# Performance work log

Hardware: AMD Instinct MI355X
Metric: run time of the kernel (lower is better)

## Reference

```python
import jax, jax.numpy as jnp
import numpy as np

ALPHA = 0.5
NEG_INF_DIAG = 1e6


def setup_inputs() -> dict:
    key = jax.random.key(0)
    k1, k2, k3, k4 = jax.random.split(key, 4)
    B, Nq, Ns, D = 64, 32, 1024, 128
    return {
        "query_single": jax.random.normal(k1, (B, D), dtype=jnp.float32),
        "doc_single": jax.random.normal(k2, (B, D), dtype=jnp.float32),
        "query_multi": jax.random.normal(k3, (B, Nq, D), dtype=jnp.float32),
        "doc_multi": jax.random.normal(k4, (B, Ns, D), dtype=jnp.float32),
    }


def _single_vector_loss(q, d):
    # q, d: (B, D) -> in-batch softmax cross-entropy with diagonal targets
    scores = jnp.einsum("bd,cd->bc", q, d)  # (B, B)
    logp = jax.nn.log_softmax(scores, axis=-1)
    return -jnp.mean(jnp.diagonal(logp))


def _multi_vector_loss(q, d):
    # q: (B, Nq, D), d: (B, Ns, D)
    # MaxSim: max over doc tokens, sum over query tokens
    sim = jnp.einsum("bnd,csd->bcns", q, d)  # (B, B, Nq, Ns) -- large intermediate
    scores = jnp.sum(jnp.max(sim, axis=3), axis=2)  # (B, B)
    pos = jnp.diagonal(scores)  # (B,)
    B = scores.shape[0]
    neg = jnp.max(scores - jnp.eye(B, dtype=scores.dtype) * NEG_INF_DIAG, axis=1)
    return jnp.mean(jax.nn.softplus(neg - pos))


def reference(query_single, doc_single, query_multi, doc_multi):
    sv_loss = _single_vector_loss(query_single, doc_single)
    mv_loss = _multi_vector_loss(query_multi, doc_multi)
    total = ALPHA * sv_loss + (1.0 - ALPHA) * mv_loss
    return sv_loss, mv_loss, total
```

## Files before the change

### kernel.cpp

```cpp
#include <hip/hip_runtime.h>


typedef __attribute__((ext_vector_type(8))) short short8;
typedef __attribute__((ext_vector_type(4))) float f32x4;

static __device__ __forceinline__ unsigned short f2bf(float f) {
  unsigned int u = __float_as_uint(f);
  u += 0x7fffu + ((u >> 16) & 1u);
  return (unsigned short)(u >> 16);
}

static __device__ __forceinline__ void g2l16(const void* g, void* l) {
  __builtin_amdgcn_global_load_lds(
      (const __attribute__((address_space(1))) unsigned int*)g,
      (__attribute__((address_space(3))) unsigned int*)l, 16, 0, 0);
}

__global__ void convert_kernel(const float* __restrict__ qm,
                               const float* __restrict__ dm,
                               unsigned char* __restrict__ dmb,
                               unsigned short* __restrict__ qmb) {
  const int NDM = 1048576;
  const int NT = NDM + 32768;
  for (int g = blockIdx.x * 256 + threadIdx.x; g < NT;
       g += gridDim.x * 256) {
    const float* src;
    unsigned char* dst;
    if (g < NDM) {
      const int c = g >> 14;
      const int r = g & 16383;
      const int s = r >> 4;
      const int kc = r & 15;
      src = dm + ((size_t)c * 131072 + (size_t)s * 128 + kc * 8);
      dst = dmb + ((size_t)c * 262144 + s * 256 +
                   ((kc * 16) ^ ((s & 7) << 4)));
    } else {
      const int gg = g - NDM;
      const int row = gg >> 4;
      const int kc = gg & 15;
      src = qm + (size_t)row * 128 + kc * 8;
      dst = (unsigned char*)(qmb + (size_t)row * 128 + kc * 8);
    }
    const float4 a = *(const float4*)src;
    const float4 b = *(const float4*)(src + 4);
    short8 w;
    w[0] = (short)f2bf(a.x); w[1] = (short)f2bf(a.y);
    w[2] = (short)f2bf(a.z); w[3] = (short)f2bf(a.w);
    w[4] = (short)f2bf(b.x); w[5] = (short)f2bf(b.y);
    w[6] = (short)f2bf(b.z); w[7] = (short)f2bf(b.w);
    *(short8*)dst = w;
  }
}

__global__ __launch_bounds__(256, 2) void mv_kernel(
    const unsigned short* __restrict__ qmb,
    const unsigned char* __restrict__ dmb,
    const float* __restrict__ qs, const float* __restrict__ ds,
    float* __restrict__ part, float* __restrict__ svp) {
  __shared__ __align__(16) unsigned char smem[34816];

  const int tid = threadIdx.x;
  const int ln = tid & 63;
  const int wv = tid >> 6;
  const int wgid = blockIdx.x;

  if (wgid >= 512) {
    const int rb = wgid - 512;
    float* dl = (float*)smem;
    for (int i = tid; i < 8192; i += 256)
      dl[(i >> 7) * 129 + (i & 127)] = ds[i];
    __syncthreads();
    const int cc = ln;
    for (int rr = 0; rr < 2; ++rr) {
      const int row = rb * 8 + wv * 2 + rr;
      const float* q = qs + (size_t)row * 128;
      float acc = 0.f;
#pragma unroll
      for (int k = 0; k < 128; ++k) acc += q[k] * dl[cc * 129 + k];
      float m = acc;
      for (int d = 1; d < 64; d <<= 1) m = fmaxf(m, __shfl_xor(m, d));
      float e = expf(acc - m);
      float ssum = e;
      for (int d = 1; d < 64; d <<= 1) ssum += __shfl_xor(ssum, d);
      const float lp = acc - m - logf(ssum);
      const float diag = __shfl(lp, row);
      if (ln == 0) svp[row] = -diag;
    }
    return;
  }

  const int rb = wgid & 3;
  const int c = (wgid >> 2) & 63;
  const int sc = wgid >> 8;

  const int lrow = ln & 15;
  const int lkg = ln >> 4;

  short8 qf[8][4];
#pragma unroll
  for (int rt = 0; rt < 8; ++rt) {
    const int row = rb * 512 + wv * 128 + rt * 16 + lrow;
    const unsigned short* qp = qmb + (size_t)row * 128 + lkg * 8;
#pragma unroll
    for (int kk = 0; kk < 4; ++kk)
      qf[rt][kk] = *(const short8*)(qp + kk * 32);
  }

  f32x4 maxv[8];
#pragma unroll
  for (int rt = 0; rt < 8; ++rt)
#pragma unroll
    for (int r = 0; r < 4; ++r) maxv[rt][r] = -3.0e38f;

  const unsigned char* dbase = dmb + (size_t)c * 262144 + (size_t)sc * 131072;
  float* rowmax = (float*)(smem + 32768);

#pragma unroll
  for (int i = 0; i < 4; ++i) {
    const int chunk = wv * 4 + i;
    g2l16(dbase + chunk * 1024 + ln * 16, smem + chunk * 1024);
  }
  __syncthreads();

  for (int t = 0; t < 8; ++t) {
    const unsigned char* cur = smem + (t & 1) * 16384;
    if (t < 7) {
      unsigned char* nxt = smem + ((t + 1) & 1) * 16384;
      const unsigned char* gsrc = dbase + (t + 1) * 16384;
#pragma unroll
      for (int i = 0; i < 4; ++i) {
        const int chunk = wv * 4 + i;
        g2l16(gsrc + chunk * 1024 + ln * 16, nxt + chunk * 1024);
      }
    }
#pragma unroll
    for (int cc = 0; cc < 4; ++cc) {
      const int s = cc * 16 + lrow;
      const unsigned char* bp = cur + s * 256;
      const int swz = (s & 7) << 4;
      short8 df[4];
#pragma unroll
      for (int kk = 0; kk < 4; ++kk)
        df[kk] = *(const short8*)(bp + ((kk * 64 + lkg * 16) ^ swz));
#pragma unroll
      for (int rt = 0; rt < 8; ++rt) {
        f32x4 a = {0.f, 0.f, 0.f, 0.f};
#pragma unroll
        for (int kk = 0; kk < 4; ++kk)
          a = __builtin_amdgcn_mfma_f32_16x16x32_bf16(qf[rt][kk], df[kk], a,
                                                      0, 0, 0);
#pragma unroll
        for (int r = 0; r < 4; ++r) maxv[rt][r] = fmaxf(maxv[rt][r], a[r]);
      }
    }
    __syncthreads();
  }

#pragma unroll
  for (int rt = 0; rt < 8; ++rt)
#pragma unroll
    for (int r = 0; r < 4; ++r) {
      float v = maxv[rt][r];
      v = fmaxf(v, __shfl_xor(v, 1));
      v = fmaxf(v, __shfl_xor(v, 2));
      v = fmaxf(v, __shfl_xor(v, 4));
      v = fmaxf(v, __shfl_xor(v, 8));
      if (lrow == 0) rowmax[wv * 128 + rt * 16 + lkg * 4 + r] = v;
    }
  __syncthreads();

  const size_t pb = (size_t)(c * 2 + sc) * 2048 + rb * 512;
  part[pb + tid] = rowmax[tid];
  part[pb + 256 + tid] = rowmax[256 + tid];
}

__global__ void reduce_kernel(const float* __restrict__ part,
                              float* __restrict__ scores) {
  const int c = blockIdx.x;
  const int t = threadIdx.x;
  const float* p0 = part + (size_t)(c * 2 + 0) * 2048;
  const float* p1 = part + (size_t)(c * 2 + 1) * 2048;
  float s = 0.f;
#pragma unroll
  for (int i = 0; i < 8; ++i) {
    const int r = t * 8 + i;
    s += fmaxf(p0[r], p1[r]);
  }
  s += __shfl_xor(s, 1);
  s += __shfl_xor(s, 2);
  if ((t & 3) == 0) scores[(t >> 2) * 64 + c] = s;
}

__global__ void final_kernel(const float* __restrict__ scores,
                             const float* __restrict__ svp,
                             float* __restrict__ out) {
  const int b = threadIdx.x;
  float sv = svp[b];
  for (int d = 1; d < 64; d <<= 1) sv += __shfl_xor(sv, d);
  sv *= (1.0f / 64.0f);

  const float pos = scores[b * 64 + b];
  float neg = -3.0e38f;
  for (int c = 0; c < 64; ++c) {
    float v = scores[b * 64 + c] - (c == b ? 1.0e6f : 0.0f);
    neg = fmaxf(neg, v);
  }
  const float t = neg - pos;
  float sp = fmaxf(t, 0.f) + log1pf(expf(-fabsf(t)));
  for (int d = 1; d < 64; d <<= 1) sp += __shfl_xor(sp, d);
  if (b == 0) {
    const float mvl = sp / 64.0f;
    out[0] = sv;
    out[1] = mvl;
    out[2] = 0.5f * sv + 0.5f * mvl;
  }
}

__global__ void sv_kernel_fb(const float* __restrict__ qs,
                             const float* __restrict__ ds,
                             float* __restrict__ out_sv) {
  __shared__ float sc[64][64];
  const int tid = threadIdx.x;
  for (int p = tid; p < 4096; p += 256) {
    const int b = p >> 6, c = p & 63;
    const float4* qa = (const float4*)(qs + b * 128);
    const float4* da = (const float4*)(ds + c * 128);
    float acc = 0.f;
#pragma unroll
    for (int i = 0; i < 32; ++i) {
      const float4 x = qa[i], y = da[i];
      acc += x.x * y.x + x.y * y.y + x.z * y.z + x.w * y.w;
    }
    sc[b][c] = acc;
  }
  __syncthreads();
  if (tid < 64) {
    float m = -3.0e38f;
    for (int c = 0; c < 64; ++c) m = fmaxf(m, sc[tid][c]);
    float s = 0.f;
    for (int c = 0; c < 64; ++c) s += expf(sc[tid][c] - m);
    float lp = sc[tid][tid] - (m + logf(s));
    for (int d = 1; d < 64; d <<= 1) lp += __shfl_xor(lp, d);
    if (tid == 0) *out_sv = -lp / 64.0f;
  }
}

__global__ __launch_bounds__(256, 4) void mv_gemm_fb(
    const float* __restrict__ qm, const float* __restrict__ dm,
    float* __restrict__ scores) {
  __shared__ unsigned char dtb[64 * 256];
  __shared__ float rowmax[128];
  const int c = blockIdx.y;
  const int rb = blockIdx.x;
  const int tid = threadIdx.x;
  const int ln = tid & 63;
  const int wv = tid >> 6;
  const int lrow = ln & 15;
  const int lkg = ln >> 4;
  short8 qf[2][4];
#pragma unroll
  for (int rt = 0; rt < 2; ++rt) {
    const int row = rb * 128 + wv * 32 + rt * 16 + lrow;
    const float* qp = qm + (size_t)row * 128 + lkg * 8;
#pragma unroll
    for (int kk = 0; kk < 4; ++kk) {
      const float4 a = *(const float4*)(qp + kk * 32);
      const float4 b = *(const float4*)(qp + kk * 32 + 4);
      short8 f;
      f[0] = (short)f2bf(a.x); f[1] = (short)f2bf(a.y);
      f[2] = (short)f2bf(a.z); f[3] = (short)f2bf(a.w);
      f[4] = (short)f2bf(b.x); f[5] = (short)f2bf(b.y);
      f[6] = (short)f2bf(b.z); f[7] = (short)f2bf(b.w);
      qf[rt][kk] = f;
    }
  }
  f32x4 maxv[2];
#pragma unroll
  for (int rt = 0; rt < 2; ++rt)
#pragma unroll
    for (int r = 0; r < 4; ++r) maxv[rt][r] = -3.0e38f;
  const float* dbase = dm + (size_t)c * 1024 * 128;
  for (int t = 0; t < 16; ++t) {
    __syncthreads();
#pragma unroll
    for (int i = 0; i < 4; ++i) {
      const int ch = tid + i * 256;
      const int s = ch >> 4;
      const int kc = ch & 15;
      const float* p = dbase + (size_t)(t * 64 + s) * 128 + kc * 8;
      const float4 a = *(const float4*)p;
      const float4 b = *(const float4*)(p + 4);
      short8 w;
      w[0] = (short)f2bf(a.x); w[1] = (short)f2bf(a.y);
      w[2] = (short)f2bf(a.z); w[3] = (short)f2bf(a.w);
      w[4] = (short)f2bf(b.x); w[5] = (short)f2bf(b.y);
      w[6] = (short)f2bf(b.z); w[7] = (short)f2bf(b.w);
      *(short8*)(dtb + s * 256 + ((kc * 16) ^ ((s & 7) << 4))) = w;
    }
    __syncthreads();
#pragma unroll
    for (int cc = 0; cc < 4; ++cc) {
      const int s = cc * 16 + lrow;
      short8 df[4];
#pragma unroll
      for (int kk = 0; kk < 4; ++kk)
        df[kk] = *(const short8*)(dtb + s * 256 +
                                  ((kk * 64 + lkg * 16) ^ ((s & 7) << 4)));
#pragma unroll
      for (int rt = 0; rt < 2; ++rt) {
        f32x4 acc = {0.f, 0.f, 0.f, 0.f};
#pragma unroll
        for (int kk = 0; kk < 4; ++kk)
          acc = __builtin_amdgcn_mfma_f32_16x16x32_bf16(qf[rt][kk], df[kk],
                                                        acc, 0, 0, 0);
#pragma unroll
        for (int r = 0; r < 4; ++r) maxv[rt][r] = fmaxf(maxv[rt][r], acc[r]);
      }
    }
  }
#pragma unroll
  for (int rt = 0; rt < 2; ++rt)
#pragma unroll
    for (int r = 0; r < 4; ++r) {
      float v = maxv[rt][r];
      v = fmaxf(v, __shfl_xor(v, 1));
      v = fmaxf(v, __shfl_xor(v, 2));
      v = fmaxf(v, __shfl_xor(v, 4));
      v = fmaxf(v, __shfl_xor(v, 8));
      maxv[rt][r] = v;
    }
  if (lrow == 0) {
#pragma unroll
    for (int rt = 0; rt < 2; ++rt)
#pragma unroll
      for (int r = 0; r < 4; ++r)
        rowmax[wv * 32 + rt * 16 + lkg * 4 + r] = maxv[rt][r];
  }
  __syncthreads();
  if (tid < 128) {
    float v = rowmax[tid];
    v += __shfl_xor(v, 1);
    v += __shfl_xor(v, 2);
    v += __shfl_xor(v, 4);
    v += __shfl_xor(v, 8);
    v += __shfl_xor(v, 16);
    if ((tid & 31) == 0) scores[(rb * 4 + (tid >> 5)) * 64 + c] = v;
  }
}

__global__ void final_fb(const float* __restrict__ scores,
                         const float* __restrict__ sv_ptr,
                         float* __restrict__ out) {
  const int b = threadIdx.x;
  const float pos = scores[b * 64 + b];
  float neg = -3.0e38f;
  for (int c = 0; c < 64; ++c) {
    float v = scores[b * 64 + c] - (c == b ? 1.0e6f : 0.0f);
    neg = fmaxf(neg, v);
  }
  const float t = neg - pos;
  float sp = fmaxf(t, 0.f) + log1pf(expf(-fabsf(t)));
  for (int d = 1; d < 64; d <<= 1) sp += __shfl_xor(sp, d);
  if (b == 0) {
    const float mvl = sp / 64.0f;
    const float sv = *sv_ptr;
    out[0] = sv;
    out[1] = mvl;
    out[2] = 0.5f * sv + 0.5f * mvl;
  }
}

extern "C" void kernel_launch(void* const* d_in, const int* in_sizes, int n_in,
                              void* d_out, int out_size, void* d_ws,
                              size_t ws_size, hipStream_t stream) {
  const float* qs = (const float*)d_in[0];
  const float* ds = (const float*)d_in[1];
  const float* qm = (const float*)d_in[2];
  const float* dm = (const float*)d_in[3];
  float* out = (float*)d_out;

  const size_t NEED = 16777216u + 524288u + 1048576u + 16384u + 256u;
  if (ws_size >= NEED) {
    unsigned char* dmb = (unsigned char*)d_ws;
    unsigned short* qmb = (unsigned short*)(dmb + 16777216u);
    float* part = (float*)(dmb + 16777216u + 524288u);
    float* scores = (float*)(dmb + 16777216u + 524288u + 1048576u);
    float* svp = scores + 4096;
    convert_kernel<<<2048, 256, 0, stream>>>(qm, dm, dmb, qmb);
    mv_kernel<<<520, 256, 0, stream>>>(qmb, dmb, qs, ds, part, svp);
    reduce_kernel<<<64, 256, 0, stream>>>(part, scores);
    final_kernel<<<1, 64, 0, stream>>>(scores, svp, out);
  } else {
    float* scores = (float*)d_ws;
    float* sv = scores + 4096;
    sv_kernel_fb<<<1, 256, 0, stream>>>(qs, ds, sv);
    mv_gemm_fb<<<dim3(16, 64), 256, 0, stream>>>(qm, dm, scores);
    final_fb<<<1, 64, 0, stream>>>(scores, sv, out);
  }
}
```

Baseline: 55.23 us.

## Fuse fp32-to-bf16 conversion into MaxSim kernel, dropping separate convert pass

Removes the standalone convert kernel that wrote a bf16 swizzled copy of the doc and query tensors to workspace. The main kernel now streams fp32 doc tiles into LDS, converts them to a bf16 swizzled double buffer in-kernel, and converts the query fragments in registers on load. This saves a kernel launch and a full write-plus-reread of the bf16 copy. In exchange each workgroup reads twice the bytes per tile, uses about 66KB of LDS (which may lower occupancy), and adds an extra barrier plus conversion work per tile.

Result: slower. 185.3 us (+235.6%).

```diff
diff --git a/kernel.cpp b/kernel.cpp
--- a/kernel.cpp
+++ b/kernel.cpp
@@ -16,48 +16,11 @@
       (__attribute__((address_space(3))) unsigned int*)l, 16, 0, 0);
 }
 
-__global__ void convert_kernel(const float* __restrict__ qm,
-                               const float* __restrict__ dm,
-                               unsigned char* __restrict__ dmb,
-                               unsigned short* __restrict__ qmb) {
-  const int NDM = 1048576;
-  const int NT = NDM + 32768;
-  for (int g = blockIdx.x * 256 + threadIdx.x; g < NT;
-       g += gridDim.x * 256) {
-    const float* src;
-    unsigned char* dst;
-    if (g < NDM) {
-      const int c = g >> 14;
-      const int r = g & 16383;
-      const int s = r >> 4;
-      const int kc = r & 15;
-      src = dm + ((size_t)c * 131072 + (size_t)s * 128 + kc * 8);
-      dst = dmb + ((size_t)c * 262144 + s * 256 +
-                   ((kc * 16) ^ ((s & 7) << 4)));
-    } else {
-      const int gg = g - NDM;
-      const int row = gg >> 4;
-      const int kc = gg & 15;
-      src = qm + (size_t)row * 128 + kc * 8;
-      dst = (unsigned char*)(qmb + (size_t)row * 128 + kc * 8);
-    }
-    const float4 a = *(const float4*)src;
-    const float4 b = *(const float4*)(src + 4);
-    short8 w;
-    w[0] = (short)f2bf(a.x); w[1] = (short)f2bf(a.y);
-    w[2] = (short)f2bf(a.z); w[3] = (short)f2bf(a.w);
-    w[4] = (short)f2bf(b.x); w[5] = (short)f2bf(b.y);
-    w[6] = (short)f2bf(b.z); w[7] = (short)f2bf(b.w);
-    *(short8*)dst = w;
-  }
-}
-
 __global__ __launch_bounds__(256, 2) void mv_kernel(
-    const unsigned short* __restrict__ qmb,
-    const unsigned char* __restrict__ dmb,
+    const float* __restrict__ qm, const float* __restrict__ dm,
     const float* __restrict__ qs, const float* __restrict__ ds,
     float* __restrict__ part, float* __restrict__ svp) {
-  __shared__ __align__(16) unsigned char smem[34816];
+  __shared__ __align__(16) unsigned char smem[67584];
 
   const int tid = threadIdx.x;
   const int ln = tid & 63;
@@ -96,14 +59,33 @@
   const int lrow = ln & 15;
   const int lkg = ln >> 4;
 
+  float* fbuf = (float*)smem;
+  float* rowmax = (float*)(smem + 65536);
+
+  const float* dmF = dm + (size_t)c * 131072 + (size_t)sc * 65536;
+
+#pragma unroll
+  for (int i = 0; i < 8; ++i) {
+    const int ch = wv * 8 + i;
+    g2l16(dmF + ch * 256 + ln * 4, smem + ch * 1024 + ln * 16);
+  }
+
   short8 qf[8][4];
 #pragma unroll
   for (int rt = 0; rt < 8; ++rt) {
     const int row = rb * 512 + wv * 128 + rt * 16 + lrow;
-    const unsigned short* qp = qmb + (size_t)row * 128 + lkg * 8;
-#pragma unroll
-    for (int kk = 0; kk < 4; ++kk)
-      qf[rt][kk] = *(const short8*)(qp + kk * 32);
+    const float* qp = qm + (size_t)row * 128 + lkg * 8;
+#pragma unroll
+    for (int kk = 0; kk < 4; ++kk) {
+      const float4 a = *(const float4*)(qp + kk * 32);
+      const float4 b = *(const float4*)(qp + kk * 32 + 4);
+      short8 f;
+      f[0] = (short)f2bf(a.x); f[1] = (short)f2bf(a.y);
+      f[2] = (short)f2bf(a.z); f[3] = (short)f2bf(a.w);
+      f[4] = (short)f2bf(b.x); f[5] = (short)f2bf(b.y);
+      f[6] = (short)f2bf(b.z); f[7] = (short)f2bf(b.w);
+      qf[rt][kk] = f;
+    }
   }
 
   f32x4 maxv[8];
@@ -112,27 +94,38 @@
 #pragma unroll
     for (int r = 0; r < 4; ++r) maxv[rt][r] = -3.0e38f;
 
-  const unsigned char* dbase = dmb + (size_t)c * 262144 + (size_t)sc * 131072;
-  float* rowmax = (float*)(smem + 32768);
-
-#pragma unroll
-  for (int i = 0; i < 4; ++i) {
-    const int chunk = wv * 4 + i;
-    g2l16(dbase + chunk * 1024 + ln * 16, smem + chunk * 1024);
-  }
   __syncthreads();
 
+  {
+    unsigned char* bb = smem + 32768;
+#pragma unroll
+    for (int i = 0; i < 4; ++i) {
+      const int ch = tid + i * 256;
+      const int s = ch >> 4;
+      const int kc = ch & 15;
+      const float* p = fbuf + s * 128 + kc * 8;
+      const float4 a = *(const float4*)p;
+      const float4 b = *(const float4*)(p + 4);
+      short8 w;
+      w[0] = (short)f2bf(a.x); w[1] = (short)f2bf(a.y);
+      w[2] = (short)f2bf(a.z); w[3] = (short)f2bf(a.w);
+      w[4] = (short)f2bf(b.x); w[5] = (short)f2bf(b.y);
+      w[6] = (short)f2bf(b.z); w[7] = (short)f2bf(b.w);
+      *(short8*)(bb + s * 256 + ((kc * 16) ^ ((s & 7) << 4))) = w;
+    }
+  }
+
   for (int t = 0; t < 8; ++t) {
-    const unsigned char* cur = smem + (t & 1) * 16384;
+    __syncthreads();
     if (t < 7) {
-      unsigned char* nxt = smem + ((t + 1) & 1) * 16384;
-      const unsigned char* gsrc = dbase + (t + 1) * 16384;
-#pragma unroll
-      for (int i = 0; i < 4; ++i) {
-        const int chunk = wv * 4 + i;
-        g2l16(gsrc + chunk * 1024 + ln * 16, nxt + chunk * 1024);
+      const float* gt = dmF + (t + 1) * 8192;
+#pragma unroll
+      for (int i = 0; i < 8; ++i) {
+        const int ch = wv * 8 + i;
+        g2l16(gt + ch * 256 + ln * 4, smem + ch * 1024 + ln * 16);
       }
     }
+    const unsigned char* cur = smem + 32768 + (t & 1) * 16384;
 #pragma unroll
     for (int cc = 0; cc < 4; ++cc) {
       const int s = cc * 16 + lrow;
@@ -154,6 +147,24 @@
       }
     }
     __syncthreads();
+    if (t < 7) {
+      unsigned char* bb = smem + 32768 + ((t + 1) & 1) * 16384;
+#pragma unroll
+      for (int i = 0; i < 4; ++i) {
+        const int ch = tid + i * 256;
+        const int s = ch >> 4;
+        const int kc = ch & 15;
+        const float* p = fbuf + s * 128 + kc * 8;
+        const float4 a = *(const float4*)p;
+        const float4 b = *(const float4*)(p + 4);
+        short8 w;
+        w[0] = (short)f2bf(a.x); w[1] = (short)f2bf(a.y);
+        w[2] = (short)f2bf(a.z); w[3] = (short)f2bf(a.w);
+        w[4] = (short)f2bf(b.x); w[5] = (short)f2bf(b.y);
+        w[6] = (short)f2bf(b.z); w[7] = (short)f2bf(b.w);
+        *(short8*)(bb + s * 256 + ((kc * 16) ^ ((s & 7) << 4))) = w;
+      }
+    }
   }
 
 #pragma unroll
@@ -379,15 +390,12 @@
   const float* dm = (const float*)d_in[3];
   float* out = (float*)d_out;
 
-  const size_t NEED = 16777216u + 524288u + 1048576u + 16384u + 256u;
+  const size_t NEED = 1048576u + 16384u + 256u;
   if (ws_size >= NEED) {
-    unsigned char* dmb = (unsigned char*)d_ws;
-    unsigned short* qmb = (unsigned short*)(dmb + 16777216u);
-    float* part = (float*)(dmb + 16777216u + 524288u);
-    float* scores = (float*)(dmb + 16777216u + 524288u + 1048576u);
+    float* part = (float*)d_ws;
+    float* scores = (float*)((unsigned char*)d_ws + 1048576u);
     float* svp = scores + 4096;
-    convert_kernel<<<2048, 256, 0, stream>>>(qm, dm, dmb, qmb);
-    mv_kernel<<<520, 256, 0, stream>>>(qmb, dmb, qs, ds, part, svp);
+    mv_kernel<<<520, 256, 0, stream>>>(qm, dm, qs, ds, part, svp);
     reduce_kernel<<<64, 256, 0, stream>>>(part, scores);
     final_kernel<<<1, 64, 0, stream>>>(scores, svp, out);
   } else {
```
